# Optimization experiments

Hardware: AMD Instinct MI355X
Metric: run time of the kernel (lower is better)

## Reference

```python
import jax, jax.numpy as jnp
import numpy as np

B, S, D, H = 4, 2048, 1024, 16
DH = D // H


def setup_inputs() -> dict:
    key = jax.random.key(0)
    k1, k2, k3, k4, k5 = jax.random.split(key, 5)
    scale = 1.0 / np.sqrt(D)
    return {
        "x": jax.random.normal(k1, (B, S, D), dtype=jnp.float32),
        "w_in": jax.random.normal(k2, (3 * D, D), dtype=jnp.float32) * scale,
        "b_in": jax.random.normal(k3, (3 * D,), dtype=jnp.float32) * 0.01,
        "w_out": jax.random.normal(k4, (D, D), dtype=jnp.float32) * scale,
        "b_out": jax.random.normal(k5, (D,), dtype=jnp.float32) * 0.01,
        "causal_mask": 1,
    }


def reference(x, w_in, b_in, w_out, b_out, causal_mask):
    batch, seq, d = x.shape
    # fused QKV projection: [B,S,3D]
    qkv = jnp.einsum('bsd,ed->bse', x, w_in) + b_in
    q, k, v = jnp.split(qkv, 3, axis=-1)
    # [B,S,H,DH]
    q = q.reshape(batch, seq, H, DH)
    k = k.reshape(batch, seq, H, DH)
    v = v.reshape(batch, seq, H, DH)
    # scaled dot-product attention, scale = 1/sqrt(d_head)
    scores = jnp.einsum('bqhd,bkhd->bhqk', q, k) / jnp.sqrt(jnp.asarray(DH, dtype=x.dtype))
    if causal_mask:  # static Python bool/int, matches is_causal semantics
        mask = jnp.tril(jnp.ones((seq, seq), dtype=bool))
        scores = jnp.where(mask, scores, jnp.asarray(-jnp.inf, dtype=scores.dtype))
    attn = jax.nn.softmax(scores, axis=-1)
    out = jnp.einsum('bhqk,bkhd->bqhd', attn, v).reshape(batch, seq, d)
    return jnp.einsum('bsd,ed->bse', out, w_out) + b_out
```

## Files before the change

kernel.cpp:

```cpp
#include <hip/hip_runtime.h>
#include <hip/hip_bf16.h>
#include <stdint.h>

constexpr int kB  = 4;
constexpr int kS  = 2048;
constexpr int kD  = 1024;
constexpr int kH  = 16;
constexpr int kDH = 64;
constexpr int kM  = kB * kS;
constexpr int k3D = 3 * kD;

constexpr float kQscale = 0.18033688011112042f;

typedef __attribute__((ext_vector_type(8))) short short8;
typedef __attribute__((ext_vector_type(4))) float f32x4;

__device__ __forceinline__ float exp2v(float x) {
  return __builtin_amdgcn_exp2f(x);
}

__device__ __forceinline__ unsigned short f2bf(float f) {
  unsigned u = __float_as_uint(f);
  u += 0x7fffu + ((u >> 16) & 1u);
  return (unsigned short)(u >> 16);
}

__device__ __forceinline__ unsigned cvtpk2bf(float lo, float hi) {
  unsigned r;
  asm("v_cvt_pk_bf16_f32 %0, %1, %2" : "=v"(r) : "v"(lo), "v"(hi));
  return r;
}

__device__ __forceinline__ void async16(const void* g, void* l) {
  __builtin_amdgcn_global_load_lds(
      (const __attribute__((address_space(1))) unsigned int*)g,
      (__attribute__((address_space(3))) unsigned int*)l, 16, 0, 0);
}

__global__ __launch_bounds__(256) void cvt_bf16_3(
    const float* __restrict__ x, const float* __restrict__ wi,
    const float* __restrict__ wo, unsigned short* __restrict__ xb,
    unsigned short* __restrict__ wib, unsigned short* __restrict__ wob) {
  constexpr int n_x  = kM * kD / 4;
  constexpr int n_wi = k3D * kD / 4;
  int i = blockIdx.x * 256 + threadIdx.x;
  const float* src;
  unsigned short* dst;
  int j;
  if (i < n_x)            { src = x;  dst = xb;  j = i; }
  else if (i < n_x + n_wi){ src = wi; dst = wib; j = i - n_x; }
  else                    { src = wo; dst = wob; j = i - n_x - n_wi; }
  float4 v = ((const float4*)src)[j];
  ushort4 r;
  r.x = f2bf(v.x); r.y = f2bf(v.y); r.z = f2bf(v.z); r.w = f2bf(v.w);
  ((ushort4*)dst)[j] = r;
}

template <bool OUT_BF16, bool QSCALE>
__global__ __launch_bounds__(512, 2) void gemm_mfma_256(
    const unsigned short* __restrict__ A, int lda,
    const unsigned short* __restrict__ Bt, int ldb,
    const float* __restrict__ bias, void* __restrict__ Cp, int ldc, int K) {
  __shared__ unsigned short Asl[2][16384];
  __shared__ unsigned short Bsl[2][16384];
  const int t = threadIdx.x;
  const int lane = t & 63, l15 = lane & 15, quad = lane >> 4, w = t >> 6;

  const int nwg = gridDim.x * gridDim.y;
  int bid = blockIdx.y * gridDim.x + blockIdx.x;
  if ((nwg & 7) == 0) bid = (bid & 7) * (nwg >> 3) + (bid >> 3);
  const int bx = bid % gridDim.x, by = bid / gridDim.x;
  const int row0 = by * 256, col0 = bx * 256;
  const int wm = (w & 1) * 128, wn = (w >> 1) * 64;

  f32x4 acc[8][4] = {};

  const unsigned short* gA[2][2];
  const unsigned short* gB[2][2];
#pragma unroll
  for (int h = 0; h < 2; ++h)
#pragma unroll
    for (int ss = 0; ss < 2; ++ss) {
      const int s = t + ss * 512;
      const int r = s >> 3, c = (s & 7) ^ (r & 7);
      gA[h][ss] = A  + (size_t)(row0 + h * 128 + r) * lda + c * 8;
      gB[h][ss] = Bt + (size_t)(col0 + h * 128 + r) * ldb + c * 8;
    }

#define STG_A(h, buf, k0)                                              \
  do {                                                                 \
    async16(gA[h][0] + (k0), Asl[buf] + (h) * 8192 + t * 8);           \
    async16(gA[h][1] + (k0), Asl[buf] + (h) * 8192 + (t + 512) * 8);   \
  } while (0)
#define STG_B(h, buf, k0)                                              \
  do {                                                                 \
    async16(gB[h][0] + (k0), Bsl[buf] + (h) * 8192 + t * 8);           \
    async16(gB[h][1] + (k0), Bsl[buf] + (h) * 8192 + (t + 512) * 8);   \
  } while (0)

#define ARD(mq, mt, ks)                                                  \
  (*(const short8*)(as + (wm + (mq) * 64 + (mt) * 16 + l15) * 64 +       \
                    ((((ks) * 4 + quad) ^ (l15 & 7)) * 8)))
#define BRD(nq, nt, ks)                                                  \
  (*(const short8*)(bs + (wn + (nq) * 32 + (nt) * 16 + l15) * 64 +       \
                    ((((ks) * 4 + quad) ^ (l15 & 7)) * 8)))

  const int nkt = K / 64;
  STG_A(0, 0, 0); STG_A(1, 0, 0); STG_B(0, 0, 0); STG_B(1, 0, 0);

  short8 af[2][4][2];
  short8 bf[2][2];

  for (int kt = 0; kt < nkt; ++kt) {
    const int buf = kt & 1, nbuf = buf ^ 1;
    const int k0n = (kt + 1) * 64;
    const bool pf = (kt + 1 < nkt);
    const unsigned short* as = Asl[buf];
    const unsigned short* bs = Bsl[buf];

    asm volatile("s_waitcnt vmcnt(0)" ::: "memory");
    __builtin_amdgcn_s_barrier();
    __builtin_amdgcn_sched_barrier(0);

    if (pf) STG_A(0, nbuf, k0n);
#pragma unroll
    for (int mt = 0; mt < 4; ++mt)
#pragma unroll
      for (int ks = 0; ks < 2; ++ks) af[0][mt][ks] = ARD(0, mt, ks);
#pragma unroll
    for (int nt = 0; nt < 2; ++nt)
#pragma unroll
      for (int ks = 0; ks < 2; ++ks) bf[nt][ks] = BRD(0, nt, ks);
    __builtin_amdgcn_s_setprio(1);
#pragma unroll
    for (int mt = 0; mt < 4; ++mt)
#pragma unroll
      for (int nt = 0; nt < 2; ++nt)
#pragma unroll
        for (int ks = 0; ks < 2; ++ks)
          acc[mt][nt] = __builtin_amdgcn_mfma_f32_16x16x32_bf16(
              af[0][mt][ks], bf[nt][ks], acc[mt][nt], 0, 0, 0);
    __builtin_amdgcn_s_setprio(0);

    if (pf) STG_A(1, nbuf, k0n);
#pragma unroll
    for (int mt = 0; mt < 4; ++mt)
#pragma unroll
      for (int ks = 0; ks < 2; ++ks) af[1][mt][ks] = ARD(1, mt, ks);
    __builtin_amdgcn_s_setprio(1);
#pragma unroll
    for (int mt = 0; mt < 4; ++mt)
#pragma unroll
      for (int nt = 0; nt < 2; ++nt)
#pragma unroll
        for (int ks = 0; ks < 2; ++ks)
          acc[4 + mt][nt] = __builtin_amdgcn_mfma_f32_16x16x32_bf16(
              af[1][mt][ks], bf[nt][ks], acc[4 + mt][nt], 0, 0, 0);
    __builtin_amdgcn_s_setprio(0);

    if (pf) STG_B(0, nbuf, k0n);
#pragma unroll
    for (int nt = 0; nt < 2; ++nt)
#pragma unroll
      for (int ks = 0; ks < 2; ++ks) bf[nt][ks] = BRD(1, nt, ks);
    __builtin_amdgcn_s_setprio(1);
#pragma unroll
    for (int mt = 0; mt < 4; ++mt)
#pragma unroll
      for (int nt = 0; nt < 2; ++nt)
#pragma unroll
        for (int ks = 0; ks < 2; ++ks)
          acc[4 + mt][2 + nt] = __builtin_amdgcn_mfma_f32_16x16x32_bf16(
              af[1][mt][ks], bf[nt][ks], acc[4 + mt][2 + nt], 0, 0, 0);
    __builtin_amdgcn_s_setprio(0);

    if (pf) STG_B(1, nbuf, k0n);
    __builtin_amdgcn_s_setprio(1);
#pragma unroll
    for (int mt = 0; mt < 4; ++mt)
#pragma unroll
      for (int nt = 0; nt < 2; ++nt)
#pragma unroll
        for (int ks = 0; ks < 2; ++ks)
          acc[mt][2 + nt] = __builtin_amdgcn_mfma_f32_16x16x32_bf16(
              af[0][mt][ks], bf[nt][ks], acc[mt][2 + nt], 0, 0, 0);
    __builtin_amdgcn_s_setprio(0);
  }
#undef STG_A
#undef STG_B
#undef ARD
#undef BRD

  const float sc = (QSCALE && col0 < kD) ? kQscale : 1.0f;
  float bv[4];
#pragma unroll
  for (int n = 0; n < 4; ++n)
    bv[n] = bias[col0 + wn + (n >> 1) * 32 + (n & 1) * 16 + l15];
#pragma unroll
  for (int m = 0; m < 8; ++m)
#pragma unroll
    for (int i = 0; i < 4; ++i) {
      const size_t r =
          (size_t)(row0 + wm + (m >> 2) * 64 + (m & 3) * 16 + quad * 4 + i);
#pragma unroll
      for (int n = 0; n < 4; ++n) {
        float v = (acc[m][n][i] + bv[n]) * sc;
        const size_t cidx =
            r * (size_t)ldc + col0 + wn + (n >> 1) * 32 + (n & 1) * 16 + l15;
        if (OUT_BF16) ((unsigned short*)Cp)[cidx] = f2bf(v);
        else          ((float*)Cp)[cidx] = v;
      }
    }
}

template <bool OUT_BF16, bool QSCALE>
__global__ __launch_bounds__(256) void gemm_mfma_128(
    const unsigned short* __restrict__ A, int lda,
    const unsigned short* __restrict__ Bt, int ldb,
    const float* __restrict__ bias, void* __restrict__ Cp, int ldc, int K) {
  __shared__ unsigned short As[2][4096];
  __shared__ unsigned short Bs[2][4096];
  const int t = threadIdx.x;
  const int lane = t & 63, l15 = lane & 15, quad = lane >> 4, w = t >> 6;

  const int nwg = gridDim.x * gridDim.y;
  int bid = blockIdx.y * gridDim.x + blockIdx.x;
  if ((nwg & 7) == 0) bid = (bid & 7) * (nwg >> 3) + (bid >> 3);
  const int bx = bid % gridDim.x, by = bid / gridDim.x;

  const int row0 = by * 128, col0 = bx * 128;
  const int wm = (w & 1) * 64, wn = (w >> 1) * 64;

  f32x4 acc[4][4] = {};

  const int q1 = t, q2 = t + 256;
  const unsigned short* a1 = A  + (size_t)(row0 + (q1 & 127)) * lda + (q1 >> 7) * 8;
  const unsigned short* a2 = A  + (size_t)(row0 + (q2 & 127)) * lda + (q2 >> 7) * 8;
  const unsigned short* b1 = Bt + (size_t)(col0 + (q1 & 127)) * ldb + (q1 >> 7) * 8;
  const unsigned short* b2 = Bt + (size_t)(col0 + (q2 & 127)) * ldb + (q2 >> 7) * 8;

  const int nIter = K / 32;
  async16(a1, As[0] + q1 * 8);
  async16(a2, As[0] + q2 * 8);
  async16(b1, Bs[0] + q1 * 8);
  async16(b2, Bs[0] + q2 * 8);

  for (int it = 0; it < nIter; ++it) {
    __syncthreads();
    const int cb = it & 1, nb = cb ^ 1;
    if (it + 1 < nIter) {
      const int k0 = (it + 1) * 32;
      async16(a1 + k0, As[nb] + q1 * 8);
      async16(a2 + k0, As[nb] + q2 * 8);
      async16(b1 + k0, Bs[nb] + q1 * 8);
      async16(b2 + k0, Bs[nb] + q2 * 8);
    }
    short8 af[4], bf[4];
#pragma unroll
    for (int mt = 0; mt < 4; ++mt)
      af[mt] = *(const short8*)(As[cb] + (quad * 128 + wm + mt * 16 + l15) * 8);
#pragma unroll
    for (int nt = 0; nt < 4; ++nt)
      bf[nt] = *(const short8*)(Bs[cb] + (quad * 128 + wn + nt * 16 + l15) * 8);
#pragma unroll
    for (int mt = 0; mt < 4; ++mt)
#pragma unroll
      for (int nt = 0; nt < 4; ++nt)
        acc[mt][nt] = __builtin_amdgcn_mfma_f32_16x16x32_bf16(
            af[mt], bf[nt], acc[mt][nt], 0, 0, 0);
  }

  const float sc = (QSCALE && col0 < kD) ? kQscale : 1.0f;
  float bv[4];
#pragma unroll
  for (int nt = 0; nt < 4; ++nt) bv[nt] = bias[col0 + wn + nt * 16 + l15];
#pragma unroll
  for (int mt = 0; mt < 4; ++mt)
#pragma unroll
    for (int i = 0; i < 4; ++i) {
      const size_t r = (size_t)(row0 + wm + mt * 16 + quad * 4 + i);
#pragma unroll
      for (int nt = 0; nt < 4; ++nt) {
        float v = (acc[mt][nt][i] + bv[nt]) * sc;
        const size_t cidx = r * (size_t)ldc + col0 + wn + nt * 16 + l15;
        if (OUT_BF16) ((unsigned short*)Cp)[cidx] = f2bf(v);
        else          ((float*)Cp)[cidx] = v;
      }
    }
}

__global__ __launch_bounds__(256) void v_transpose(
    const unsigned short* __restrict__ qkvb, unsigned short* __restrict__ vtb) {
  __shared__ unsigned short L[64][72];
  const int kt = blockIdx.x, h = blockIdx.y, b = blockIdx.z;
  const int t = threadIdx.x;
  const unsigned short* src = qkvb + (size_t)(b * kS) * k3D + 2 * kD + h * kDH;
#pragma unroll
  for (int p = 0; p < 2; ++p) {
    const int q = t + p * 256;
    const int r = q >> 3, c = q & 7;
    *(short8*)(&L[r][c * 8]) =
        *(const short8*)(src + (size_t)(kt * 64 + r) * k3D + c * 8);
  }
  __syncthreads();
  unsigned short* dst = vtb + (size_t)((b * kH + h) * kDH) * kS + kt * 64;
  const int key2 = (t & 31) * 2, dg = t >> 5;
#pragma unroll
  for (int i = 0; i < 8; ++i) {
    const int d = dg * 8 + i;
    ushort2 v = make_ushort2(L[key2][d], L[key2 + 1][d]);
    *(ushort2*)(dst + (size_t)d * kS + key2) = v;
  }
}

__global__ __launch_bounds__(256, 4) void flash_attn_mfma(
    unsigned short* __restrict__ qkvb, const unsigned short* __restrict__ vtb,
    const int* __restrict__ cflag) {
  __shared__ unsigned short QP[4096];
  __shared__ unsigned short Ks[2][4096];
  __shared__ unsigned short Vt[2][4096];

  const int lin = blockIdx.x;
  const int pr = lin >> 6;
  const int g  = ((lin >> 3) & 7) * 8 + (lin & 7);
  const int h = g & 15, b = g >> 4;
  const int t = threadIdx.x;
  const int lane = t & 63, l15 = lane & 15, quad = lane >> 4, w = t >> 6;
  const bool causal = (*cflag) != 0;

  unsigned short* qbase = qkvb + (size_t)(b * kS) * k3D + h * kDH;
  const unsigned short* vbase = vtb + (size_t)((b * kH + h) * kDH) * kS;
  const int c0 = t, c1 = t + 256;

  for (int half = 0; half < 2; ++half) {
    const int qt = half ? (31 - pr) : pr;
    const int q0 = qt * 64;
    const int ntiles = causal ? (qt + 1) : 32;

    async16(qbase + (size_t)(q0 + (c0 & 63)) * k3D + (c0 >> 6) * 8, QP + c0 * 8);
    async16(qbase + (size_t)(q0 + (c1 & 63)) * k3D + (c1 >> 6) * 8, QP + c1 * 8);
    async16(qbase + kD + (size_t)(c0 & 63) * k3D + (c0 >> 6) * 8, Ks[0] + c0 * 8);
    async16(qbase + kD + (size_t)(c1 & 63) * k3D + (c1 >> 6) * 8, Ks[0] + c1 * 8);
    async16(vbase + (size_t)(c0 & 63) * kS + (c0 >> 6) * 8, Vt[0] + c0 * 8);
    async16(vbase + (size_t)(c1 & 63) * kS + (c1 >> 6) * 8, Vt[0] + c1 * 8);
    __syncthreads();

    short8 bq[2];
#pragma unroll
    for (int kf = 0; kf < 2; ++kf)
      bq[kf] = *(const short8*)(
          QP + ((kf * 4 + quad) * 64 + w * 16 + l15) * 8);

    f32x4 O[4] = {};
    float m_i = -3.0e38f, l_i = 0.f;

    for (int kt = 0; kt < ntiles; ++kt) {
      const int cb = kt & 1, nb = cb ^ 1;
      const int kk0 = kt * 64;

      if (kt + 1 < ntiles) {
        const int kn = kk0 + 64;
        async16(qbase + kD + (size_t)(kn + (c0 & 63)) * k3D + (c0 >> 6) * 8,
                Ks[nb] + c0 * 8);
        async16(qbase + kD + (size_t)(kn + (c1 & 63)) * k3D + (c1 >> 6) * 8,
                Ks[nb] + c1 * 8);
        async16(vbase + (size_t)(c0 & 63) * kS + kn + (c0 >> 6) * 8,
                Vt[nb] + c0 * 8);
        async16(vbase + (size_t)(c1 & 63) * kS + kn + (c1 >> 6) * 8,
                Vt[nb] + c1 * 8);
      }

      f32x4 s[4];
      __builtin_amdgcn_s_setprio(1);
#pragma unroll
      for (int mt = 0; mt < 4; ++mt) {
        short8 a0 = *(const short8*)(Ks[cb] + ((quad)*64 + mt * 16 + l15) * 8);
        short8 a1 =
            *(const short8*)(Ks[cb] + ((4 + quad) * 64 + mt * 16 + l15) * 8);
        f32x4 z = {};
        z = __builtin_amdgcn_mfma_f32_16x16x32_bf16(a0, bq[0], z, 0, 0, 0);
        z = __builtin_amdgcn_mfma_f32_16x16x32_bf16(a1, bq[1], z, 0, 0, 0);
        s[mt] = z;
      }
      __builtin_amdgcn_s_setprio(0);

      const int gq = q0 + w * 16 + l15;
      if (causal && kt == ntiles - 1) {
#pragma unroll
        for (int mt = 0; mt < 4; ++mt)
#pragma unroll
          for (int i = 0; i < 4; ++i)
            if (kk0 + mt * 16 + quad * 4 + i > gq) s[mt][i] = -3.0e38f;
      }
      float mx = -3.0e38f;
#pragma unroll
      for (int mt = 0; mt < 4; ++mt)
#pragma unroll
        for (int i = 0; i < 4; ++i) mx = fmaxf(mx, s[mt][i]);
      mx = fmaxf(mx, __shfl_xor(mx, 16));
      mx = fmaxf(mx, __shfl_xor(mx, 32));

      if (!__all(mx <= m_i + 8.0f)) {
        const float mn = fmaxf(m_i, mx);
        const float alpha = exp2v(m_i - mn);
        m_i = mn;
        l_i *= alpha;
#pragma unroll
        for (int i = 0; i < 4; ++i) {
          const float a = __shfl(alpha, quad * 4 + i);
#pragma unroll
          for (int ntd = 0; ntd < 4; ++ntd) O[ntd][i] *= a;
        }
      }

      float p[4][4];
      float rs = 0.f;
#pragma unroll
      for (int mt = 0; mt < 4; ++mt)
#pragma unroll
        for (int i = 0; i < 4; ++i) {
          p[mt][i] = exp2v(s[mt][i] - m_i);
          rs += p[mt][i];
        }
      rs += __shfl_xor(rs, 16);
      rs += __shfl_xor(rs, 32);
      l_i += rs;

#pragma unroll
      for (int mt = 0; mt < 4; ++mt) {
        uint2 pk = make_uint2(cvtpk2bf(p[mt][0], p[mt][1]),
                              cvtpk2bf(p[mt][2], p[mt][3]));
        *(uint2*)(QP + ((mt * 2 + (quad >> 1)) * 64 + w * 16 + l15) * 8 +
                  (quad & 1) * 4) = pk;
      }

      __builtin_amdgcn_s_setprio(1);
#pragma unroll
      for (int kf = 0; kf < 2; ++kf) {
        short8 aP = *(const short8*)(
            QP + ((kf * 4 + quad) * 64 + w * 16 + l15) * 8);
#pragma unroll
        for (int ntd = 0; ntd < 4; ++ntd) {
          short8 bV = *(const short8*)(
              Vt[cb] + ((kf * 4 + quad) * 64 + ntd * 16 + l15) * 8);
          O[ntd] = __builtin_amdgcn_mfma_f32_16x16x32_bf16(
              aP, bV, O[ntd], 0, 0, 0);
        }
      }
      __builtin_amdgcn_s_setprio(0);

      __syncthreads();
    }

#pragma unroll
    for (int i = 0; i < 4; ++i) {
      const float linv = 1.0f / __shfl(l_i, quad * 4 + i);
      unsigned short* dst =
          qbase + (size_t)(q0 + w * 16 + quad * 4 + i) * k3D;
#pragma unroll
      for (int ntd = 0; ntd < 4; ++ntd)
        dst[ntd * 16 + l15] = f2bf(O[ntd][i] * linv);
    }
  }
}

extern "C" void kernel_launch(void* const* d_in, const int* in_sizes, int n_in,
                              void* d_out, int out_size, void* d_ws,
                              size_t ws_size, hipStream_t stream) {
  const float* x     = (const float*)d_in[0];
  const float* w_in  = (const float*)d_in[1];
  const float* b_in  = (const float*)d_in[2];
  const float* w_out = (const float*)d_in[3];
  const float* b_out = (const float*)d_in[4];
  const int*   cfl   = (const int*)d_in[5];
  float* out = (float*)d_out;

  char* ws = (char*)d_ws;
  unsigned short* qkvb = (unsigned short*)(ws);
  unsigned short* xb   = (unsigned short*)(ws + 50331648);
  unsigned short* wib  = (unsigned short*)(ws + 67108864);
  unsigned short* wob  = (unsigned short*)(ws + 73400320);
  unsigned short* vtb  = (unsigned short*)(ws + 75497472);

  cvt_bf16_3<<<(kM * kD + k3D * kD + kD * kD) / 4 / 256, 256, 0, stream>>>(
      x, w_in, w_out, xb, wib, wob);

  gemm_mfma_256<true, true><<<dim3(k3D / 256, kM / 256), 512, 0, stream>>>(
      xb, kD, wib, kD, b_in, qkvb, k3D, kD);

  v_transpose<<<dim3(kS / 64, kH, kB), 256, 0, stream>>>(qkvb, vtb);

  flash_attn_mfma<<<dim3(16 * kH * kB), 256, 0, stream>>>(qkvb, vtb, cfl);

  gemm_mfma_128<false, false><<<dim3(kD / 128, kM / 128), 256, 0, stream>>>(
      qkvb, k3D, wob, kD, b_out, out, kD, kD);
}
```

Baseline: 300.3 us.

## Software-pipeline attention loop: compute next QK^T during softmax, split K/V staging

Restructures the flash-attention inner loop so the QK^T MFMAs for tile kt+1 are issued while tile kt's softmax and PV run. K and V loads are now staged separately, with K prefetched two tiles ahead. The single __syncthreads is replaced by manual vmcnt waits and s_barrier calls. The aim is to hide softmax latency and LDS/global load latency behind matrix work. In exchange it raises register pressure and depends on fragile hand-counted vmcnt values, which could break correctness or occupancy.

```diff
diff --git a/kernel.cpp b/kernel.cpp
--- a/kernel.cpp
+++ b/kernel.cpp
@@ -332,6 +332,34 @@
   const unsigned short* vbase = vtb + (size_t)((b * kH + h) * kDH) * kS;
   const int c0 = t, c1 = t + 256;
 
+#define STG_K(kn, buf)                                                       \
+  do {                                                                       \
+    async16(qbase + kD + (size_t)((kn) + (c0 & 63)) * k3D + (c0 >> 6) * 8,   \
+            Ks[buf] + c0 * 8);                                               \
+    async16(qbase + kD + (size_t)((kn) + (c1 & 63)) * k3D + (c1 >> 6) * 8,   \
+            Ks[buf] + c1 * 8);                                               \
+  } while (0)
+#define STG_V(kn, buf)                                                       \
+  do {                                                                       \
+    async16(vbase + (size_t)(c0 & 63) * kS + (kn) + (c0 >> 6) * 8,           \
+            Vt[buf] + c0 * 8);                                               \
+    async16(vbase + (size_t)(c1 & 63) * kS + (kn) + (c1 >> 6) * 8,           \
+            Vt[buf] + c1 * 8);                                               \
+  } while (0)
+#define QKT(dst, kbuf)                                                       \
+  do {                                                                       \
+    _Pragma("unroll")                                                        \
+    for (int mt = 0; mt < 4; ++mt) {                                         \
+      short8 a0_ = *(const short8*)((kbuf) + ((quad)*64 + mt * 16 + l15) * 8);\
+      short8 a1_ =                                                           \
+          *(const short8*)((kbuf) + ((4 + quad) * 64 + mt * 16 + l15) * 8);  \
+      f32x4 z_ = {};                                                         \
+      z_ = __builtin_amdgcn_mfma_f32_16x16x32_bf16(a0_, bq[0], z_, 0, 0, 0); \
+      z_ = __builtin_amdgcn_mfma_f32_16x16x32_bf16(a1_, bq[1], z_, 0, 0, 0); \
+      dst[mt] = z_;                                                          \
+    }                                                                        \
+  } while (0)
+
   for (int half = 0; half < 2; ++half) {
     const int qt = half ? (31 - pr) : pr;
     const int q0 = qt * 64;
@@ -339,10 +367,7 @@
 
     async16(qbase + (size_t)(q0 + (c0 & 63)) * k3D + (c0 >> 6) * 8, QP + c0 * 8);
     async16(qbase + (size_t)(q0 + (c1 & 63)) * k3D + (c1 >> 6) * 8, QP + c1 * 8);
-    async16(qbase + kD + (size_t)(c0 & 63) * k3D + (c0 >> 6) * 8, Ks[0] + c0 * 8);
-    async16(qbase + kD + (size_t)(c1 & 63) * k3D + (c1 >> 6) * 8, Ks[0] + c1 * 8);
-    async16(vbase + (size_t)(c0 & 63) * kS + (c0 >> 6) * 8, Vt[0] + c0 * 8);
-    async16(vbase + (size_t)(c1 & 63) * kS + (c1 >> 6) * 8, Vt[0] + c1 * 8);
+    STG_K(0, 0);
     __syncthreads();
 
     short8 bq[2];
@@ -351,38 +376,29 @@
       bq[kf] = *(const short8*)(
           QP + ((kf * 4 + quad) * 64 + w * 16 + l15) * 8);
 
+    if (ntiles > 1) STG_K(64, 1);
+    STG_V(0, 0);
+
+    f32x4 s[4];
+    QKT(s, Ks[0]);
+    __builtin_amdgcn_s_barrier();
+
     f32x4 O[4] = {};
     float m_i = -3.0e38f, l_i = 0.f;
 
     for (int kt = 0; kt < ntiles; ++kt) {
-      const int cb = kt & 1, nb = cb ^ 1;
+      const int kb_next = (kt + 1) & 1;
       const int kk0 = kt * 64;
 
+      if (kt + 2 < ntiles) STG_K(kk0 + 128, kt & 1);
+
       if (kt + 1 < ntiles) {
-        const int kn = kk0 + 64;
-        async16(qbase + kD + (size_t)(kn + (c0 & 63)) * k3D + (c0 >> 6) * 8,
-                Ks[nb] + c0 * 8);
-        async16(qbase + kD + (size_t)(kn + (c1 & 63)) * k3D + (c1 >> 6) * 8,
-                Ks[nb] + c1 * 8);
-        async16(vbase + (size_t)(c0 & 63) * kS + kn + (c0 >> 6) * 8,
-                Vt[nb] + c0 * 8);
-        async16(vbase + (size_t)(c1 & 63) * kS + kn + (c1 >> 6) * 8,
-                Vt[nb] + c1 * 8);
-      }
-
-      f32x4 s[4];
-      __builtin_amdgcn_s_setprio(1);
-#pragma unroll
-      for (int mt = 0; mt < 4; ++mt) {
-        short8 a0 = *(const short8*)(Ks[cb] + ((quad)*64 + mt * 16 + l15) * 8);
-        short8 a1 =
-            *(const short8*)(Ks[cb] + ((4 + quad) * 64 + mt * 16 + l15) * 8);
-        f32x4 z = {};
-        z = __builtin_amdgcn_mfma_f32_16x16x32_bf16(a0, bq[0], z, 0, 0, 0);
-        z = __builtin_amdgcn_mfma_f32_16x16x32_bf16(a1, bq[1], z, 0, 0, 0);
-        s[mt] = z;
-      }
-      __builtin_amdgcn_s_setprio(0);
+        if (kt + 2 < ntiles) asm volatile("s_waitcnt vmcnt(4)" ::: "memory");
+        else                 asm volatile("s_waitcnt vmcnt(2)" ::: "memory");
+      }
+      __builtin_amdgcn_s_barrier();
+
+      if (kt + 1 < ntiles) STG_V(kk0 + 64, kb_next);
 
       const int gq = q0 + w * 16 + l15;
       if (causal && kt == ntiles - 1) {
@@ -434,6 +450,18 @@
                   (quad & 1) * 4) = pk;
       }
 
+      f32x4 s2[4];
+      if (kt + 1 < ntiles) {
+        __builtin_amdgcn_s_setprio(1);
+        QKT(s2, Ks[kb_next]);
+        __builtin_amdgcn_s_setprio(0);
+      }
+
+      if (kt + 2 < ntiles)      asm volatile("s_waitcnt vmcnt(4)" ::: "memory");
+      else if (kt + 1 < ntiles) asm volatile("s_waitcnt vmcnt(2)" ::: "memory");
+      else                      asm volatile("s_waitcnt vmcnt(0)" ::: "memory");
+      __builtin_amdgcn_s_barrier();
+
       __builtin_amdgcn_s_setprio(1);
 #pragma unroll
       for (int kf = 0; kf < 2; ++kf) {
@@ -442,15 +470,19 @@
 #pragma unroll
         for (int ntd = 0; ntd < 4; ++ntd) {
           short8 bV = *(const short8*)(
-              Vt[cb] + ((kf * 4 + quad) * 64 + ntd * 16 + l15) * 8);
+              Vt[kt & 1] + ((kf * 4 + quad) * 64 + ntd * 16 + l15) * 8);
           O[ntd] = __builtin_amdgcn_mfma_f32_16x16x32_bf16(
               aP, bV, O[ntd], 0, 0, 0);
         }
       }
       __builtin_amdgcn_s_setprio(0);
 
-      __syncthreads();
+      if (kt + 1 < ntiles) {
+        s[0] = s2[0]; s[1] = s2[1]; s[2] = s2[2]; s[3] = s2[3];
+      }
     }
+
+    __builtin_amdgcn_s_barrier();
 
 #pragma unroll
     for (int i = 0; i < 4; ++i) {
@@ -462,6 +494,9 @@
         dst[ntd * 16 + l15] = f2bf(O[ntd][i] * linv);
     }
   }
+#undef STG_K
+#undef STG_V
+#undef QKT
 }
 
 extern "C" void kernel_launch(void* const* d_in, const int* in_sizes, int n_in,
```

Measured after the change: 306.4 us. +2.0%, slower.

## Fuse V transpose into QKV GEMM epilogue via swizzled LDS staging

Applied to the files above, without the earlier changes.

The QKV projection GEMM now writes the V-column tiles straight into the transposed vtb layout. It stages the bf16 results in shared memory with an XOR swizzle, then stores 16-byte rows along the sequence dimension. This removes the separate v_transpose kernel, one launch, and the round trip of writing V into qkvb and reading it back. The cost is extra LDS traffic and two barriers in the epilogue of the V-column blocks, and V is no longer written into qkvb.

```diff
diff --git a/kernel.cpp b/kernel.cpp
--- a/kernel.cpp
+++ b/kernel.cpp
@@ -56,13 +56,15 @@
   ((ushort4*)dst)[j] = r;
 }
 
-template <bool OUT_BF16, bool QSCALE>
+template <bool OUT_BF16, bool QSCALE, bool VT>
 __global__ __launch_bounds__(512, 2) void gemm_mfma_256(
     const unsigned short* __restrict__ A, int lda,
     const unsigned short* __restrict__ Bt, int ldb,
-    const float* __restrict__ bias, void* __restrict__ Cp, int ldc, int K) {
-  __shared__ unsigned short Asl[2][16384];
-  __shared__ unsigned short Bsl[2][16384];
+    const float* __restrict__ bias, void* __restrict__ Cp, int ldc, int K,
+    unsigned short* __restrict__ vtbp) {
+  __shared__ unsigned short SL[65536];
+  auto Asl = (unsigned short(*)[16384])(SL);
+  auto Bsl = (unsigned short(*)[16384])(SL + 32768);
   const int t = threadIdx.x;
   const int lane = t & 63, l15 = lane & 15, quad = lane >> 4, w = t >> 6;
 
@@ -191,11 +193,43 @@
 #undef ARD
 #undef BRD
 
-  const float sc = (QSCALE && col0 < kD) ? kQscale : 1.0f;
   float bv[4];
 #pragma unroll
   for (int n = 0; n < 4; ++n)
     bv[n] = bias[col0 + wn + (n >> 1) * 32 + (n & 1) * 16 + l15];
+
+  if (VT && col0 >= 2 * kD) {
+    __syncthreads();
+#pragma unroll
+    for (int m = 0; m < 8; ++m)
+#pragma unroll
+      for (int n = 0; n < 4; ++n) {
+        const int cl = wn + (n >> 1) * 32 + (n & 1) * 16 + l15;
+        const int u = (wm >> 2) + (m >> 2) * 16 + (m & 3) * 4 + quad;
+        uint2 pk = make_uint2(
+            cvtpk2bf(acc[m][n][0] + bv[n], acc[m][n][1] + bv[n]),
+            cvtpk2bf(acc[m][n][2] + bv[n], acc[m][n][3] + bv[n]));
+        *(uint2*)(SL + cl * 256 + ((u ^ (cl & 15)) << 2)) = pk;
+      }
+    __syncthreads();
+    const int b_ = by >> 3, s0 = (by & 7) * 256;
+    const int lhalf = lane >> 5, l31 = lane & 31;
+#pragma unroll
+    for (int ps = 0; ps < 16; ++ps) {
+      const int cl = ps * 16 + w * 2 + lhalf;
+      uint2 v0 = *(const uint2*)(SL + cl * 256 +
+                                 (((l31 * 2) ^ (cl & 15)) << 2));
+      uint2 v1 = *(const uint2*)(SL + cl * 256 +
+                                 (((l31 * 2 + 1) ^ (cl & 15)) << 2));
+      uint4 vv = make_uint4(v0.x, v0.y, v1.x, v1.y);
+      unsigned short* gd =
+          vtbp + (size_t)(b_ * 1024 + col0 - 2 * kD + cl) * kS + s0 + l31 * 8;
+      *(uint4*)gd = vv;
+    }
+    return;
+  }
+
+  const float sc = (QSCALE && col0 < kD) ? kQscale : 1.0f;
 #pragma unroll
   for (int m = 0; m < 8; ++m)
 #pragma unroll
@@ -287,30 +321,6 @@
         else          ((float*)Cp)[cidx] = v;
       }
     }
-}
-
-__global__ __launch_bounds__(256) void v_transpose(
-    const unsigned short* __restrict__ qkvb, unsigned short* __restrict__ vtb) {
-  __shared__ unsigned short L[64][72];
-  const int kt = blockIdx.x, h = blockIdx.y, b = blockIdx.z;
-  const int t = threadIdx.x;
-  const unsigned short* src = qkvb + (size_t)(b * kS) * k3D + 2 * kD + h * kDH;
-#pragma unroll
-  for (int p = 0; p < 2; ++p) {
-    const int q = t + p * 256;
-    const int r = q >> 3, c = q & 7;
-    *(short8*)(&L[r][c * 8]) =
-        *(const short8*)(src + (size_t)(kt * 64 + r) * k3D + c * 8);
-  }
-  __syncthreads();
-  unsigned short* dst = vtb + (size_t)((b * kH + h) * kDH) * kS + kt * 64;
-  const int key2 = (t & 31) * 2, dg = t >> 5;
-#pragma unroll
-  for (int i = 0; i < 8; ++i) {
-    const int d = dg * 8 + i;
-    ushort2 v = make_ushort2(L[key2][d], L[key2 + 1][d]);
-    *(ushort2*)(dst + (size_t)d * kS + key2) = v;
-  }
 }
 
 __global__ __launch_bounds__(256, 4) void flash_attn_mfma(
@@ -485,10 +495,8 @@
   cvt_bf16_3<<<(kM * kD + k3D * kD + kD * kD) / 4 / 256, 256, 0, stream>>>(
       x, w_in, w_out, xb, wib, wob);
 
-  gemm_mfma_256<true, true><<<dim3(k3D / 256, kM / 256), 512, 0, stream>>>(
-      xb, kD, wib, kD, b_in, qkvb, k3D, kD);
-
-  v_transpose<<<dim3(kS / 64, kH, kB), 256, 0, stream>>>(qkvb, vtb);
+  gemm_mfma_256<true, true, true><<<dim3(k3D / 256, kM / 256), 512, 0, stream>>>(
+      xb, kD, wib, kD, b_in, qkvb, k3D, kD, vtb);
 
   flash_attn_mfma<<<dim3(16 * kH * kB), 256, 0, stream>>>(qkvb, vtb, cfl);
 
```

Measured after the change: 271.2 us. 9.7% less time.
